# Kernel optimization log

Measured on AMD Instinct MI355X. Metric: run time of the kernel, lower is better.

## Reference

```python
import jax, jax.numpy as jnp
import numpy as np

TEMPERATURE = 0.5
EPS = 1e-8  # torch CosineSimilarity eps


def setup_inputs() -> dict:
    key = jax.random.key(0)
    # x holds 2*batch_size concatenated embeddings (two augmented views)
    x = jax.random.normal(key, (4096, 512), dtype=jnp.float32)
    return {"x": x}


def reference(x) -> jnp.ndarray:
    n2 = x.shape[0]          # 2N rows
    n = n2 // 2
    # cosine similarity: normalize rows (clamped norm as in torch), then GEMM
    norms = jnp.maximum(jnp.linalg.norm(x, axis=1, keepdims=True), EPS)
    xn = x / norms
    sim = jnp.einsum('id,jd->ij', xn, xn) / TEMPERATURE  # [2N, 2N]
    # positive logit for row i is sim[i, (i+N) mod 2N]
    idx = jnp.arange(n2)
    pos = sim[idx, (idx + n) % n2]
    # CE with label 0 over logits = [pos, negatives]; since the logit set for
    # row i is exactly {sim[i, j] : j != i}, CE_i = logsumexp_{j!=i} sim[i,j] - pos_i
    sim_masked = jnp.where(jnp.eye(n2, dtype=bool), -jnp.inf, sim)
    lse = jax.nn.logsumexp(sim_masked, axis=1)
    # criterion uses reduction='sum' then divides by bsz -> mean
    return jnp.mean(lse - pos)
```

## Files before the change

### kernel.cpp

```cpp
#include <hip/hip_runtime.h>
#include <hip/hip_bf16.h>
#include <math.h>

typedef __bf16 bf16_t;
typedef __bf16 bf16x8 __attribute__((ext_vector_type(8)));
typedef float f32x4 __attribute__((ext_vector_type(4)));

#define N2 4096
#define NHALF 2048
#define DIM 512
#define TEMP_INV 2.0f

__global__ __launch_bounds__(256) void k_prep(const float* __restrict__ x,
                                              bf16_t* __restrict__ xn,
                                              float* __restrict__ pos,
                                              float* __restrict__ diag,
                                              float* __restrict__ rowsum) {
    const int pair = blockIdx.x * 4 + (threadIdx.x >> 6);
    const int lane = threadIdx.x & 63;
    const int rowi = pair;
    const int rowp = pair + NHALF;

    const float4* xi = reinterpret_cast<const float4*>(x + (size_t)rowi * DIM);
    const float4* xp = reinterpret_cast<const float4*>(x + (size_t)rowp * DIM);
    float4 a0 = xi[lane * 2], a1 = xi[lane * 2 + 1];
    float4 b0 = xp[lane * 2], b1 = xp[lane * 2 + 1];

    float ssi = a0.x*a0.x + a0.y*a0.y + a0.z*a0.z + a0.w*a0.w
              + a1.x*a1.x + a1.y*a1.y + a1.z*a1.z + a1.w*a1.w;
    float ssp = b0.x*b0.x + b0.y*b0.y + b0.z*b0.z + b0.w*b0.w
              + b1.x*b1.x + b1.y*b1.y + b1.z*b1.z + b1.w*b1.w;
    float dot = a0.x*b0.x + a0.y*b0.y + a0.z*b0.z + a0.w*b0.w
              + a1.x*b1.x + a1.y*b1.y + a1.z*b1.z + a1.w*b1.w;
#pragma unroll
    for (int off = 32; off; off >>= 1) {
        ssi += __shfl_xor(ssi, off, 64);
        ssp += __shfl_xor(ssp, off, 64);
        dot += __shfl_xor(dot, off, 64);
    }
    const float ni = fmaxf(sqrtf(ssi), 1e-8f);
    const float np = fmaxf(sqrtf(ssp), 1e-8f);
    const float sci = 1.0f / ni, scp = 1.0f / np;

    float va[8] = {a0.x, a0.y, a0.z, a0.w, a1.x, a1.y, a1.z, a1.w};
    float vb[8] = {b0.x, b0.y, b0.z, b0.w, b1.x, b1.y, b1.z, b1.w};
    bf16x8 oi, op;
    float dii = 0.0f, dpp = 0.0f;
#pragma unroll
    for (int t = 0; t < 8; ++t) {
        oi[t] = (bf16_t)(va[t] * sci);
        op[t] = (bf16_t)(vb[t] * scp);
        float fi = (float)oi[t], fp_ = (float)op[t];
        dii += fi * fi;
        dpp += fp_ * fp_;
    }
    *reinterpret_cast<bf16x8*>(xn + (size_t)rowi * DIM + lane * 8) = oi;
    *reinterpret_cast<bf16x8*>(xn + (size_t)rowp * DIM + lane * 8) = op;
#pragma unroll
    for (int off = 32; off; off >>= 1) {
        dii += __shfl_xor(dii, off, 64);
        dpp += __shfl_xor(dpp, off, 64);
    }
    if (lane == 0) {
        const float pv = TEMP_INV * dot * sci * scp;
        pos[rowi] = pv;
        pos[rowp] = pv;
        diag[rowi] = TEMP_INV * dii;
        diag[rowp] = TEMP_INV * dpp;
    }
    if (threadIdx.x < 8) rowsum[blockIdx.x * 8 + threadIdx.x] = 0.0f;
}

__device__ __forceinline__ void load_lds16(const bf16_t* g, bf16_t* l) {
    __builtin_amdgcn_global_load_lds(
        (const __attribute__((address_space(1))) unsigned int*)g,
        (__attribute__((address_space(3))) unsigned int*)l,
        16, 0, 0);
}

__global__ __launch_bounds__(256) void k_simgemm(const bf16_t* __restrict__ xn,
                                                 float* __restrict__ rowsum) {
    __shared__ bf16_t As[128 * 32];
    __shared__ bf16_t Bs[128 * 32];
    __shared__ float  rpA[128];
    __shared__ float  rpB[128];

    const int t = blockIdx.x;
    int bn = (int)((sqrtf(8.0f * (float)t + 1.0f) - 1.0f) * 0.5f);
    while ((bn * (bn + 1)) / 2 > t) --bn;
    while (((bn + 1) * (bn + 2)) / 2 <= t) ++bn;
    const int bm = t - (bn * (bn + 1)) / 2;
    const bool diagb = (bm == bn);

    const int tid  = threadIdx.x;
    const int lane = tid & 63;
    const int wid  = tid >> 6;
    const int wr   = wid >> 1;
    const int wc   = wid & 1;
    const int q    = lane >> 4;
    const int l15  = lane & 15;

    if (tid < 128) { rpA[tid] = 0.0f; rpB[tid] = 0.0f; }

    const int sRow = tid >> 2;
    const int sCol = (tid & 3) * 8;
    const bf16_t* gA0 = xn + (size_t)(bm * 128 + sRow) * DIM + sCol;
    const bf16_t* gB0 = xn + (size_t)(bn * 128 + sRow) * DIM + sCol;
    bf16_t* lA0 = &As[tid * 8];
    bf16_t* lA1 = &As[2048 + tid * 8];
    bf16_t* lB0 = &Bs[tid * 8];
    bf16_t* lB1 = &Bs[2048 + tid * 8];

    f32x4 acc[4][4] = {};

    for (int k0 = 0; k0 < DIM; k0 += 32) {
        __syncthreads();
        load_lds16(gA0 + k0, lA0);
        load_lds16(gA0 + (size_t)64 * DIM + k0, lA1);
        load_lds16(gB0 + k0, lB0);
        load_lds16(gB0 + (size_t)64 * DIM + k0, lB1);
        __syncthreads();

        bf16x8 af[4], bf[4];
#pragma unroll
        for (int mt = 0; mt < 4; ++mt)
            af[mt] = *reinterpret_cast<const bf16x8*>(
                &As[(wr * 64 + mt * 16 + l15) * 32 + q * 8]);
#pragma unroll
        for (int nt = 0; nt < 4; ++nt)
            bf[nt] = *reinterpret_cast<const bf16x8*>(
                &Bs[(wc * 64 + nt * 16 + l15) * 32 + q * 8]);
#pragma unroll
        for (int mt = 0; mt < 4; ++mt)
#pragma unroll
            for (int nt = 0; nt < 4; ++nt)
                acc[mt][nt] = __builtin_amdgcn_mfma_f32_16x16x32_bf16(
                    af[mt], bf[nt], acc[mt][nt], 0, 0, 0);
    }

    float colacc[4] = {0.0f, 0.0f, 0.0f, 0.0f};
#pragma unroll
    for (int mt = 0; mt < 4; ++mt) {
        float rowp[4] = {0.0f, 0.0f, 0.0f, 0.0f};
#pragma unroll
        for (int nt = 0; nt < 4; ++nt)
#pragma unroll
            for (int r = 0; r < 4; ++r) {
                float e = __expf(TEMP_INV * acc[mt][nt][r]);
                rowp[r] += e;
                colacc[nt] += e;
            }
#pragma unroll
        for (int r = 0; r < 4; ++r) {
            float p = rowp[r];
            p += __shfl_xor(p, 1, 64);
            p += __shfl_xor(p, 2, 64);
            p += __shfl_xor(p, 4, 64);
            p += __shfl_xor(p, 8, 64);
            if (l15 == 0) atomicAdd(&rpA[wr * 64 + mt * 16 + q * 4 + r], p);
        }
    }
    if (!diagb) {
#pragma unroll
        for (int nt = 0; nt < 4; ++nt) {
            float c = colacc[nt];
            c += __shfl_xor(c, 16, 64);
            c += __shfl_xor(c, 32, 64);
            if (q == 0) atomicAdd(&rpB[wc * 64 + nt * 16 + l15], c);
        }
    }
    __syncthreads();
    if (tid < 128) {
        atomicAdd(&rowsum[bm * 128 + tid], rpA[tid]);
    } else if (!diagb) {
        atomicAdd(&rowsum[bn * 128 + (tid - 128)], rpB[tid - 128]);
    }
}

__global__ __launch_bounds__(256) void k_finalize(const float* __restrict__ rowsum,
                                                  const float* __restrict__ pos,
                                                  const float* __restrict__ diag,
                                                  float* __restrict__ out) {
    __shared__ float red[256];
    float s = 0.0f;
    for (int i = threadIdx.x; i < N2; i += 256)
        s += __logf(rowsum[i] - __expf(diag[i])) - pos[i];
    red[threadIdx.x] = s;
    __syncthreads();
    for (int st = 128; st; st >>= 1) {
        if (threadIdx.x < st) red[threadIdx.x] += red[threadIdx.x + st];
        __syncthreads();
    }
    if (threadIdx.x == 0) out[0] = red[0] / (float)N2;
}

extern "C" void kernel_launch(void* const* d_in, const int* in_sizes, int n_in,
                              void* d_out, int out_size, void* d_ws, size_t ws_size,
                              hipStream_t stream) {
    (void)in_sizes; (void)n_in; (void)out_size; (void)ws_size;
    const float* x = (const float*)d_in[0];
    float* out = (float*)d_out;

    char* ws = (char*)d_ws;
    bf16_t* xn     = (bf16_t*)ws;
    float*  rowsum = (float*)(ws + (size_t)N2 * DIM * 2);
    float*  pos    = rowsum + N2;
    float*  diag   = pos + N2;

    k_prep<<<512, 256, 0, stream>>>(x, xn, pos, diag, rowsum);
    k_simgemm<<<528, 256, 0, stream>>>(xn, rowsum);
    k_finalize<<<1, 256, 0, stream>>>(rowsum, pos, diag, out);
}
```

Before: 82.42 us.

## Use 128x64 triangular tiles and fuse finalize via last-block counter

The similarity GEMM switches from 128x128 upper-triangular tiles (528 blocks) to 128x64 tiles over the triangle (1056 blocks), so work spreads across more CUs with smaller per-block register and LDS use, and launch bounds now allow 4 blocks per SM. The separate finalize kernel is removed. Its reduction runs in the last block to finish, detected with a global atomic counter that the prep kernel resets. The cost is more redundant A-tile loads and a fence and atomic per block.

Measured after the change: 161.1 us. 1.95x slower.

```diff
diff --git a/kernel.cpp b/kernel.cpp
--- a/kernel.cpp
+++ b/kernel.cpp
@@ -10,12 +10,14 @@
 #define NHALF 2048
 #define DIM 512
 #define TEMP_INV 2.0f
+#define NBLK 1056
 
 __global__ __launch_bounds__(256) void k_prep(const float* __restrict__ x,
                                               bf16_t* __restrict__ xn,
                                               float* __restrict__ pos,
                                               float* __restrict__ diag,
-                                              float* __restrict__ rowsum) {
+                                              float* __restrict__ rowsum,
+                                              unsigned int* __restrict__ counter) {
     const int pair = blockIdx.x * 4 + (threadIdx.x >> 6);
     const int lane = threadIdx.x & 63;
     const int rowi = pair;
@@ -38,9 +40,8 @@
         ssp += __shfl_xor(ssp, off, 64);
         dot += __shfl_xor(dot, off, 64);
     }
-    const float ni = fmaxf(sqrtf(ssi), 1e-8f);
-    const float np = fmaxf(sqrtf(ssp), 1e-8f);
-    const float sci = 1.0f / ni, scp = 1.0f / np;
+    const float sci = 1.0f / fmaxf(sqrtf(ssi), 1e-8f);
+    const float scp = 1.0f / fmaxf(sqrtf(ssp), 1e-8f);
 
     float va[8] = {a0.x, a0.y, a0.z, a0.w, a1.x, a1.y, a1.z, a1.w};
     float vb[8] = {b0.x, b0.y, b0.z, b0.w, b1.x, b1.y, b1.z, b1.w};
@@ -69,6 +70,7 @@
         diag[rowp] = TEMP_INV * dpp;
     }
     if (threadIdx.x < 8) rowsum[blockIdx.x * 8 + threadIdx.x] = 0.0f;
+    if (blockIdx.x == 0 && threadIdx.x == 8) *counter = 0u;
 }
 
 __device__ __forceinline__ void load_lds16(const bf16_t* g, bf16_t* l) {
@@ -78,19 +80,25 @@
         16, 0, 0);
 }
 
-__global__ __launch_bounds__(256) void k_simgemm(const bf16_t* __restrict__ xn,
-                                                 float* __restrict__ rowsum) {
+__global__ __launch_bounds__(256, 4) void k_simgemm(const bf16_t* __restrict__ xn,
+                                                    float* __restrict__ rowsum,
+                                                    const float* __restrict__ pos,
+                                                    const float* __restrict__ diag,
+                                                    unsigned int* __restrict__ counter,
+                                                    float* __restrict__ out) {
     __shared__ bf16_t As[128 * 32];
-    __shared__ bf16_t Bs[128 * 32];
+    __shared__ bf16_t Bs[64 * 32];
     __shared__ float  rpA[128];
-    __shared__ float  rpB[128];
+    __shared__ float  rpB[64];
+    __shared__ float  red[256];
+    __shared__ int    lastFlag;
 
     const int t = blockIdx.x;
-    int bn = (int)((sqrtf(8.0f * (float)t + 1.0f) - 1.0f) * 0.5f);
-    while ((bn * (bn + 1)) / 2 > t) --bn;
-    while (((bn + 1) * (bn + 2)) / 2 <= t) ++bn;
-    const int bm = t - (bn * (bn + 1)) / 2;
-    const bool diagb = (bm == bn);
+    int i = (int)((65.0f - sqrtf(4225.0f - 4.0f * (float)t)) * 0.5f);
+    while (i * (65 - i) > t) --i;
+    while ((i + 1) * (64 - i) <= t) ++i;
+    const int j = 2 * i + (t - i * (65 - i));
+    const bool diagc = (j <= 2 * i + 1);
 
     const int tid  = threadIdx.x;
     const int lane = tid & 63;
@@ -100,50 +108,49 @@
     const int q    = lane >> 4;
     const int l15  = lane & 15;
 
-    if (tid < 128) { rpA[tid] = 0.0f; rpB[tid] = 0.0f; }
+    if (tid < 128) rpA[tid] = 0.0f;
+    if (tid < 64)  rpB[tid] = 0.0f;
 
     const int sRow = tid >> 2;
     const int sCol = (tid & 3) * 8;
-    const bf16_t* gA0 = xn + (size_t)(bm * 128 + sRow) * DIM + sCol;
-    const bf16_t* gB0 = xn + (size_t)(bn * 128 + sRow) * DIM + sCol;
+    const bf16_t* gA0 = xn + (size_t)(i * 128 + sRow) * DIM + sCol;
+    const bf16_t* gB0 = xn + (size_t)(j * 64 + sRow) * DIM + sCol;
     bf16_t* lA0 = &As[tid * 8];
     bf16_t* lA1 = &As[2048 + tid * 8];
     bf16_t* lB0 = &Bs[tid * 8];
-    bf16_t* lB1 = &Bs[2048 + tid * 8];
-
-    f32x4 acc[4][4] = {};
+
+    f32x4 acc[4][2] = {};
 
     for (int k0 = 0; k0 < DIM; k0 += 32) {
         __syncthreads();
         load_lds16(gA0 + k0, lA0);
         load_lds16(gA0 + (size_t)64 * DIM + k0, lA1);
         load_lds16(gB0 + k0, lB0);
-        load_lds16(gB0 + (size_t)64 * DIM + k0, lB1);
         __syncthreads();
 
-        bf16x8 af[4], bf[4];
+        bf16x8 af[4], bfv[2];
 #pragma unroll
         for (int mt = 0; mt < 4; ++mt)
             af[mt] = *reinterpret_cast<const bf16x8*>(
                 &As[(wr * 64 + mt * 16 + l15) * 32 + q * 8]);
 #pragma unroll
-        for (int nt = 0; nt < 4; ++nt)
-            bf[nt] = *reinterpret_cast<const bf16x8*>(
-                &Bs[(wc * 64 + nt * 16 + l15) * 32 + q * 8]);
+        for (int nt = 0; nt < 2; ++nt)
+            bfv[nt] = *reinterpret_cast<const bf16x8*>(
+                &Bs[(wc * 32 + nt * 16 + l15) * 32 + q * 8]);
 #pragma unroll
         for (int mt = 0; mt < 4; ++mt)
 #pragma unroll
-            for (int nt = 0; nt < 4; ++nt)
+            for (int nt = 0; nt < 2; ++nt)
                 acc[mt][nt] = __builtin_amdgcn_mfma_f32_16x16x32_bf16(
-                    af[mt], bf[nt], acc[mt][nt], 0, 0, 0);
-    }
-
-    float colacc[4] = {0.0f, 0.0f, 0.0f, 0.0f};
+                    af[mt], bfv[nt], acc[mt][nt], 0, 0, 0);
+    }
+
+    float colacc[2] = {0.0f, 0.0f};
 #pragma unroll
     for (int mt = 0; mt < 4; ++mt) {
         float rowp[4] = {0.0f, 0.0f, 0.0f, 0.0f};
 #pragma unroll
-        for (int nt = 0; nt < 4; ++nt)
+        for (int nt = 0; nt < 2; ++nt)
 #pragma unroll
             for (int r = 0; r < 4; ++r) {
                 float e = __expf(TEMP_INV * acc[mt][nt][r]);
@@ -160,38 +167,46 @@
             if (l15 == 0) atomicAdd(&rpA[wr * 64 + mt * 16 + q * 4 + r], p);
         }
     }
-    if (!diagb) {
-#pragma unroll
-        for (int nt = 0; nt < 4; ++nt) {
+    if (!diagc) {
+#pragma unroll
+        for (int nt = 0; nt < 2; ++nt) {
             float c = colacc[nt];
             c += __shfl_xor(c, 16, 64);
             c += __shfl_xor(c, 32, 64);
-            if (q == 0) atomicAdd(&rpB[wc * 64 + nt * 16 + l15], c);
+            if (q == 0) atomicAdd(&rpB[wc * 32 + nt * 16 + l15], c);
         }
     }
     __syncthreads();
     if (tid < 128) {
-        atomicAdd(&rowsum[bm * 128 + tid], rpA[tid]);
-    } else if (!diagb) {
-        atomicAdd(&rowsum[bn * 128 + (tid - 128)], rpB[tid - 128]);
-    }
-}
-
-__global__ __launch_bounds__(256) void k_finalize(const float* __restrict__ rowsum,
-                                                  const float* __restrict__ pos,
-                                                  const float* __restrict__ diag,
-                                                  float* __restrict__ out) {
-    __shared__ float red[256];
-    float s = 0.0f;
-    for (int i = threadIdx.x; i < N2; i += 256)
-        s += __logf(rowsum[i] - __expf(diag[i])) - pos[i];
-    red[threadIdx.x] = s;
+        atomicAdd(&rowsum[i * 128 + tid], rpA[tid]);
+    } else if (!diagc && tid < 192) {
+        atomicAdd(&rowsum[j * 64 + (tid - 128)], rpB[tid - 128]);
+    }
+
+    __threadfence();
     __syncthreads();
-    for (int st = 128; st; st >>= 1) {
-        if (threadIdx.x < st) red[threadIdx.x] += red[threadIdx.x + st];
+    if (tid == 0) {
+        unsigned int done = __hip_atomic_fetch_add(counter, 1u, __ATOMIC_ACQ_REL,
+                                                   __HIP_MEMORY_SCOPE_AGENT);
+        lastFlag = (done == (unsigned int)(gridDim.x - 1)) ? 1 : 0;
+    }
+    __syncthreads();
+    if (lastFlag) {
+        __threadfence();
+        float s = 0.0f;
+        for (int r = tid; r < N2; r += 256) {
+            float S = __hip_atomic_load(&rowsum[r], __ATOMIC_RELAXED,
+                                        __HIP_MEMORY_SCOPE_AGENT);
+            s += __logf(S - __expf(diag[r])) - pos[r];
+        }
+        red[tid] = s;
         __syncthreads();
-    }
-    if (threadIdx.x == 0) out[0] = red[0] / (float)N2;
+        for (int st = 128; st; st >>= 1) {
+            if (tid < st) red[tid] += red[tid + st];
+            __syncthreads();
+        }
+        if (tid == 0) out[0] = red[0] / (float)N2;
+    }
 }
 
 extern "C" void kernel_launch(void* const* d_in, const int* in_sizes, int n_in,
@@ -206,8 +221,8 @@
     float*  rowsum = (float*)(ws + (size_t)N2 * DIM * 2);
     float*  pos    = rowsum + N2;
     float*  diag   = pos + N2;
-
-    k_prep<<<512, 256, 0, stream>>>(x, xn, pos, diag, rowsum);
-    k_simgemm<<<528, 256, 0, stream>>>(xn, rowsum);
-    k_finalize<<<1, 256, 0, stream>>>(rowsum, pos, diag, out);
-}
+    unsigned int* counter = (unsigned int*)(diag + N2);
+
+    k_prep<<<512, 256, 0, stream>>>(x, xn, pos, diag, rowsum, counter);
+    k_simgemm<<<NBLK, 256, 0, stream>>>(xn, rowsum, pos, diag, counter, out);
+}
```

## Load GEMM operands directly from global into registers with double buffering

Applied to the files above, without the earlier changes.

Removes the LDS staging of A and B tiles in the similarity GEMM. Each wave now loads its MFMA fragments straight from global memory into registers and uses a two-stage register double buffer across K steps, with no block-level barriers inside the loop. This avoids LDS traffic and the per-iteration synchronization. In exchange, each wave fetches operand rows that other waves in the block also fetch, relying on L1/L2 to absorb the duplication, and the per-lane 16-byte loads are strided by a full row.

After: 112.2 us. 36.2% more time.

```diff
diff --git a/kernel.cpp b/kernel.cpp
--- a/kernel.cpp
+++ b/kernel.cpp
@@ -38,9 +38,8 @@
         ssp += __shfl_xor(ssp, off, 64);
         dot += __shfl_xor(dot, off, 64);
     }
-    const float ni = fmaxf(sqrtf(ssi), 1e-8f);
-    const float np = fmaxf(sqrtf(ssp), 1e-8f);
-    const float sci = 1.0f / ni, scp = 1.0f / np;
+    const float sci = 1.0f / fmaxf(sqrtf(ssi), 1e-8f);
+    const float scp = 1.0f / fmaxf(sqrtf(ssp), 1e-8f);
 
     float va[8] = {a0.x, a0.y, a0.z, a0.w, a1.x, a1.y, a1.z, a1.w};
     float vb[8] = {b0.x, b0.y, b0.z, b0.w, b1.x, b1.y, b1.z, b1.w};
@@ -71,19 +70,10 @@
     if (threadIdx.x < 8) rowsum[blockIdx.x * 8 + threadIdx.x] = 0.0f;
 }
 
-__device__ __forceinline__ void load_lds16(const bf16_t* g, bf16_t* l) {
-    __builtin_amdgcn_global_load_lds(
-        (const __attribute__((address_space(1))) unsigned int*)g,
-        (__attribute__((address_space(3))) unsigned int*)l,
-        16, 0, 0);
-}
-
 __global__ __launch_bounds__(256) void k_simgemm(const bf16_t* __restrict__ xn,
                                                  float* __restrict__ rowsum) {
-    __shared__ bf16_t As[128 * 32];
-    __shared__ bf16_t Bs[128 * 32];
-    __shared__ float  rpA[128];
-    __shared__ float  rpB[128];
+    __shared__ float rpA[128];
+    __shared__ float rpB[128];
 
     const int t = blockIdx.x;
     int bn = (int)((sqrtf(8.0f * (float)t + 1.0f) - 1.0f) * 0.5f);
@@ -102,41 +92,46 @@
 
     if (tid < 128) { rpA[tid] = 0.0f; rpB[tid] = 0.0f; }
 
-    const int sRow = tid >> 2;
-    const int sCol = (tid & 3) * 8;
-    const bf16_t* gA0 = xn + (size_t)(bm * 128 + sRow) * DIM + sCol;
-    const bf16_t* gB0 = xn + (size_t)(bn * 128 + sRow) * DIM + sCol;
-    bf16_t* lA0 = &As[tid * 8];
-    bf16_t* lA1 = &As[2048 + tid * 8];
-    bf16_t* lB0 = &Bs[tid * 8];
-    bf16_t* lB1 = &Bs[2048 + tid * 8];
+    const bf16_t* Ab = xn + (size_t)(bm * 128 + wr * 64 + l15) * DIM + q * 8;
+    const bf16_t* Bb = xn + (size_t)(bn * 128 + wc * 64 + l15) * DIM + q * 8;
 
     f32x4 acc[4][4] = {};
-
-    for (int k0 = 0; k0 < DIM; k0 += 32) {
-        __syncthreads();
-        load_lds16(gA0 + k0, lA0);
-        load_lds16(gA0 + (size_t)64 * DIM + k0, lA1);
-        load_lds16(gB0 + k0, lB0);
-        load_lds16(gB0 + (size_t)64 * DIM + k0, lB1);
-        __syncthreads();
-
-        bf16x8 af[4], bf[4];
-#pragma unroll
-        for (int mt = 0; mt < 4; ++mt)
-            af[mt] = *reinterpret_cast<const bf16x8*>(
-                &As[(wr * 64 + mt * 16 + l15) * 32 + q * 8]);
-#pragma unroll
-        for (int nt = 0; nt < 4; ++nt)
-            bf[nt] = *reinterpret_cast<const bf16x8*>(
-                &Bs[(wc * 64 + nt * 16 + l15) * 32 + q * 8]);
+    bf16x8 a0[4], b0[4], a1[4], b1[4];
+
+#pragma unroll
+    for (int mt = 0; mt < 4; ++mt) {
+        a0[mt] = *reinterpret_cast<const bf16x8*>(Ab + (size_t)(mt * 16) * DIM);
+        b0[mt] = *reinterpret_cast<const bf16x8*>(Bb + (size_t)(mt * 16) * DIM);
+    }
+
+    for (int k0 = 0; k0 < DIM; k0 += 64) {
+#pragma unroll
+        for (int mt = 0; mt < 4; ++mt) {
+            a1[mt] = *reinterpret_cast<const bf16x8*>(Ab + (size_t)(mt * 16) * DIM + k0 + 32);
+            b1[mt] = *reinterpret_cast<const bf16x8*>(Bb + (size_t)(mt * 16) * DIM + k0 + 32);
+        }
 #pragma unroll
         for (int mt = 0; mt < 4; ++mt)
 #pragma unroll
             for (int nt = 0; nt < 4; ++nt)
                 acc[mt][nt] = __builtin_amdgcn_mfma_f32_16x16x32_bf16(
-                    af[mt], bf[nt], acc[mt][nt], 0, 0, 0);
-    }
+                    a0[mt], b0[nt], acc[mt][nt], 0, 0, 0);
+        if (k0 + 64 < DIM) {
+#pragma unroll
+            for (int mt = 0; mt < 4; ++mt) {
+                a0[mt] = *reinterpret_cast<const bf16x8*>(Ab + (size_t)(mt * 16) * DIM + k0 + 64);
+                b0[mt] = *reinterpret_cast<const bf16x8*>(Bb + (size_t)(mt * 16) * DIM + k0 + 64);
+            }
+        }
+#pragma unroll
+        for (int mt = 0; mt < 4; ++mt)
+#pragma unroll
+            for (int nt = 0; nt < 4; ++nt)
+                acc[mt][nt] = __builtin_amdgcn_mfma_f32_16x16x32_bf16(
+                    a1[mt], b1[nt], acc[mt][nt], 0, 0, 0);
+    }
+
+    __syncthreads();
 
     float colacc[4] = {0.0f, 0.0f, 0.0f, 0.0f};
 #pragma unroll
```
